# Kernel tuning notes

Hardware: AMD Instinct MI355X
Metric: run time of the kernel (lower is better)

## Reference

```python
import jax, jax.numpy as jnp
import numpy as np

N_NODES = 50000
N_EDGES = 600000
D_IN = 128      # input_dim
D_EDGE = 128    # edge_dim
GAMMA, ZETA = -0.1, 1.1  # hard-concrete stretch params


def _spectral_norm(w):
    # torch spectral_norm divides weight by its top singular value
    s = np.linalg.svd(w, compute_uv=False)[0]
    return w / s


def setup_inputs() -> dict:
    key = jax.random.key(0)
    ks = jax.random.split(key, 8)
    node_feat = jax.random.normal(ks[0], (N_NODES, D_IN), dtype=jnp.float32)
    edge_index = jax.random.randint(ks[1], (2, N_EDGES), 0, N_NODES, dtype=jnp.int64)
    rng = np.random.default_rng(0)
    # kaiming-normal init then spectral normalization (applied once at setup)
    def kaiming(fan_in, shape):
        return (rng.standard_normal(shape) * np.sqrt(2.0 / fan_in)).astype(np.float32)
    W1 = jnp.asarray(_spectral_norm(kaiming(2 * D_IN + 1, (D_EDGE, 2 * D_IN + 1))))
    W2 = jnp.asarray(_spectral_norm(kaiming(D_EDGE, (D_EDGE, D_EDGE))))
    W3 = jnp.asarray(_spectral_norm(kaiming(D_EDGE, (1, D_EDGE))))
    b1 = jnp.zeros((D_EDGE,), jnp.float32)
    b2 = jnp.zeros((D_EDGE,), jnp.float32)
    b3 = jnp.zeros((1,), jnp.float32)
    return {"node_feat": node_feat, "edge_index": edge_index,
            "W1": W1, "b1": b1, "W2": W2, "b2": b2, "W3": W3, "b3": b3}


def reference(node_feat, edge_index, W1, b1, W2, b2, W3, b3):
    # L2-normalize node features
    nf = node_feat / (jnp.linalg.norm(node_feat, axis=-1, keepdims=True) + 1e-8)
    src, tgt = edge_index[0], edge_index[1]
    hs = nf[src]                      # [E, D_IN] gather
    ht = nf[tgt]                      # [E, D_IN] gather
    dist = jnp.linalg.norm(hs - ht, axis=-1)  # [E]
    edge_features = jnp.concatenate([hs, ht, dist[:, None]], axis=-1)  # [E, 2D+1]
    h = jax.nn.relu(edge_features @ W1.T + b1)
    h = jax.nn.relu(h @ W2.T + b2)
    logAlpha = (h @ W3.T + b3).squeeze(-1)    # [E]
    # hard-concrete deterministic (l0_test) gate
    edge_weights = jnp.clip(jax.nn.sigmoid(logAlpha) * (ZETA - GAMMA) + GAMMA, 0.0, 1.0)
    return edge_weights, logAlpha
```

## Files before the change

### kernel.cpp

```cpp
#include <hip/hip_runtime.h>


#define E_TOT 600000
#define NN    50000
#define DIN   128

typedef short bf16x8 __attribute__((ext_vector_type(8)));
typedef float f32x4  __attribute__((ext_vector_type(4)));

union FragU { uint4 q; unsigned int u[4]; bf16x8 v; };

__device__ __forceinline__ unsigned int f2bf(float x) {
  unsigned int b = __float_as_uint(x);
  return ((b + 0x7fffu + ((b >> 16) & 1u)) >> 16) & 0xffffu;
}

__global__ __launch_bounds__(256) void k_norm(const float* __restrict__ nf,
                                              unsigned short* __restrict__ nfb) {
  const int wv = threadIdx.x >> 6, l = threadIdx.x & 63;
  const int h = l >> 5, r = l & 31;
  const int node = blockIdx.x * 8 + wv * 2 + h;
  const float4* row = (const float4*)(nf + (size_t)node * DIN);
  float4 v = row[r];
  float ss = v.x * v.x + v.y * v.y + v.z * v.z + v.w * v.w;
  #pragma unroll
  for (int msk = 1; msk < 32; msk <<= 1) ss += __shfl_xor(ss, msk);
  const float inv = 1.0f / (sqrtf(ss) + 1e-8f);
  uint2 o;
  o.x = f2bf(v.x * inv) | (f2bf(v.y * inv) << 16);
  o.y = f2bf(v.z * inv) | (f2bf(v.w * inv) << 16);
  ((uint2*)(nfb + (size_t)node * DIN))[r] = o;
}

__global__ __launch_bounds__(256) void k_prep(const float* __restrict__ W1,
                                              const float* __restrict__ W2,
                                              unsigned int* __restrict__ B1,
                                              unsigned int* __restrict__ B2) {
  const int id = blockIdx.x * 256 + threadIdx.x;
  if (id < 16384) {
    const int dw = id & 3, lane = (id >> 2) & 63, nt = (id >> 8) & 7, s = id >> 11;
    const int n = nt * 16 + (lane & 15);
    const int k0 = (lane >> 4) * 8 + s * 32 + dw * 2;
    B1[id] = f2bf(W1[n * 257 + k0]) | (f2bf(W1[n * 257 + k0 + 1]) << 16);
  } else {
    const int i2 = id - 16384;
    const int dw = i2 & 3, lane = (i2 >> 2) & 63, nt = (i2 >> 8) & 7, s = i2 >> 11;
    const int n = nt * 16 + (lane & 15);
    const int k0 = (lane >> 4) * 8 + s * 32 + dw * 2;
    B2[i2] = f2bf(W2[n * 128 + k0]) | (f2bf(W2[n * 128 + k0 + 1]) << 16);
  }
}

__global__ __launch_bounds__(256, 4) void k_main(
    const unsigned short* __restrict__ nfb, const int* __restrict__ ei,
    const unsigned int* __restrict__ B1, const unsigned int* __restrict__ B2,
    const float* __restrict__ W1, const float* __restrict__ b1,
    const float* __restrict__ b2, const float* __restrict__ W3,
    const float* __restrict__ b3, float* __restrict__ out) {
  __shared__ unsigned int lds[2048 + 4 * 1024];
  const int tid = threadIdx.x;
  const int wv = tid >> 6, l = tid & 63, m = l & 15, a = l >> 4;
  char* sHb = (char*)(lds + 2048) + wv * 4096;

  bool is64 = true;
  #pragma unroll
  for (int w = 1; w < 64; w += 2) is64 = is64 && (ei[w] == 0);

  const int e = blockIdx.x * 64 + wv * 16 + m;
  int nsrc, ntgt;
  if (is64) { nsrc = ei[2 * e]; ntgt = ei[2 * (E_TOT + e)]; }
  else      { nsrc = ei[e];     ntgt = ei[E_TOT + e]; }
  nsrc = min(max(nsrc, 0), NN - 1);
  ntgt = min(max(ntgt, 0), NN - 1);

  const uint4* rs = (const uint4*)(nfb + (size_t)nsrc * DIN);
  const uint4* rt = (const uint4*)(nfb + (size_t)ntgt * DIN);
  uint4 hsv[4], htv[4];
  #pragma unroll
  for (int s = 0; s < 4; ++s) { hsv[s] = rs[a + 4 * s]; htv[s] = rt[a + 4 * s]; }

  float dp = 0.f;
  #pragma unroll
  for (int i = 0; i < 4; ++i) {
    const unsigned int* hu = (const unsigned int*)&hsv[i];
    const unsigned int* tu = (const unsigned int*)&htv[i];
    #pragma unroll
    for (int j = 0; j < 4; ++j) {
      float h0 = __uint_as_float(hu[j] << 16), t0 = __uint_as_float(tu[j] << 16);
      float h1v = __uint_as_float(hu[j] & 0xffff0000u), t1v = __uint_as_float(tu[j] & 0xffff0000u);
      float d0 = h0 - t0, d1 = h1v - t1v;
      dp = fmaf(d0, d0, dp);
      dp = fmaf(d1, d1, dp);
    }
  }
  dp += __shfl_xor(dp, 16);
  dp += __shfl_xor(dp, 32);
  const float dist = sqrtf(dp);
  float dist_r[4];
  #pragma unroll
  for (int r = 0; r < 4; ++r) dist_r[r] = __shfl(dist, a * 4 + r);

  f32x4 acc[8];
  #pragma unroll
  for (int nt = 0; nt < 8; ++nt) acc[nt] = (f32x4){0.f, 0.f, 0.f, 0.f};

  const uint4* g1 = (const uint4*)B1;
  const uint4* g2 = (const uint4*)B2;
  uint4* sB = (uint4*)lds;
  uint4 n0 = g1[tid], n1 = g1[tid + 256];

  #pragma unroll
  for (int st = 0; st < 12; ++st) {
    __syncthreads();
    sB[tid] = n0; sB[tid + 256] = n1;
    __syncthreads();
    if (st < 11) {
      const int s2 = st + 1;
      if (s2 < 8) { n0 = g1[s2 * 512 + tid]; n1 = g1[s2 * 512 + tid + 256]; }
      else        { const int s3 = s2 - 8;
                    n0 = g2[s3 * 512 + tid]; n1 = g2[s3 * 512 + tid + 256]; }
    }

    FragU af;
    if (st < 4)      af.q = hsv[st];
    else if (st < 8) af.q = htv[st - 4];
    else {
      const int s2 = st - 8;
      const int col = 16 * a + 64 * s2;
      af.q = *(const uint4*)(sHb + m * 256 + (col ^ ((m & 7) << 4)));
    }

    #pragma unroll
    for (int nt = 0; nt < 8; ++nt) {
      FragU bfr; bfr.q = sB[nt * 64 + l];
      acc[nt] = __builtin_amdgcn_mfma_f32_16x16x32_bf16(af.v, bfr.v, acc[nt], 0, 0, 0);
    }

    if (st == 7) {
      #pragma unroll
      for (int nt = 0; nt < 8; ++nt) {
        const int n = nt * 16 + m;
        const float b1v = b1[n];
        const float w1l = W1[n * 257 + 256];
        #pragma unroll
        for (int r = 0; r < 4; ++r) {
          const int row = 4 * a + r;
          float v = acc[nt][r] + b1v + w1l * dist_r[r];
          v = fmaxf(v, 0.f);
          *(unsigned short*)(sHb + row * 256 + ((n * 2) ^ ((row & 7) << 4))) =
              (unsigned short)f2bf(v);
        }
        acc[nt] = (f32x4){0.f, 0.f, 0.f, 0.f};
      }
    }
  }

  float part[4] = {0.f, 0.f, 0.f, 0.f};
  #pragma unroll
  for (int nt = 0; nt < 8; ++nt) {
    const int n = nt * 16 + m;
    const float b2v = b2[n];
    const float w3v = W3[n];
    #pragma unroll
    for (int r = 0; r < 4; ++r) {
      const float h2 = fmaxf(acc[nt][r] + b2v, 0.f);
      part[r] = fmaf(h2, w3v, part[r]);
    }
  }
  #pragma unroll
  for (int r = 0; r < 4; ++r) {
    part[r] += __shfl_xor(part[r], 1);
    part[r] += __shfl_xor(part[r], 2);
    part[r] += __shfl_xor(part[r], 4);
    part[r] += __shfl_xor(part[r], 8);
  }
  if (m == 0) {
    const float b3v = b3[0];
    #pragma unroll
    for (int r = 0; r < 4; ++r) {
      const int eo = blockIdx.x * 64 + wv * 16 + a * 4 + r;
      const float la = part[r] + b3v;
      const float sg = 1.f / (1.f + __expf(-la));
      out[eo] = fminf(fmaxf(sg * 1.2f - 0.1f, 0.f), 1.f);
      out[E_TOT + eo] = la;
    }
  }
}

extern "C" void kernel_launch(void* const* d_in, const int* in_sizes, int n_in,
                              void* d_out, int out_size, void* d_ws, size_t ws_size,
                              hipStream_t stream) {
  const float* node_feat = (const float*)d_in[0];
  const int*   edge_idx  = (const int*)d_in[1];
  const float* W1 = (const float*)d_in[2];
  const float* b1 = (const float*)d_in[3];
  const float* W2 = (const float*)d_in[4];
  const float* b2 = (const float*)d_in[5];
  const float* W3 = (const float*)d_in[6];
  const float* b3 = (const float*)d_in[7];
  float* out = (float*)d_out;

  unsigned char* ws = (unsigned char*)d_ws;
  unsigned short* nfb = (unsigned short*)(ws);
  unsigned int*   B1  = (unsigned int*)(ws + 12800000);
  unsigned int*   B2  = (unsigned int*)(ws + 12800000 + 65536);

  hipLaunchKernelGGL(k_norm, dim3(6250), dim3(256), 0, stream, node_feat, nfb);
  hipLaunchKernelGGL(k_prep, dim3(96), dim3(256), 0, stream, W1, W2, B1, B2);
  hipLaunchKernelGGL(k_main, dim3(9375), dim3(256), 0, stream,
                     nfb, edge_idx, B1, B2, W1, b1, b2, W3, b3, out);
}
```

Before: 202.2 us.

## Process two edge tiles per wave with async double-buffered weight staging

Each wave now handles 32 edges (two 16-row MFMA tiles), so every staged weight fragment in LDS feeds twice as many MFMAs. Weight staging switches from register round-trips to global_load_lds async copies into a double buffer, which drops one barrier per stage. The norm and weight-prep kernels are merged into a single launch, and the 64-bit index detection becomes a wave vote. In exchange, register and LDS use grow, occupancy is bounded at 3 blocks, and the grid halves with a tail guard.

```diff
diff --git a/kernel.cpp b/kernel.cpp
--- a/kernel.cpp
+++ b/kernel.cpp
@@ -15,125 +15,156 @@
   return ((b + 0x7fffu + ((b >> 16) & 1u)) >> 16) & 0xffffu;
 }
 
-__global__ __launch_bounds__(256) void k_norm(const float* __restrict__ nf,
-                                              unsigned short* __restrict__ nfb) {
-  const int wv = threadIdx.x >> 6, l = threadIdx.x & 63;
-  const int h = l >> 5, r = l & 31;
-  const int node = blockIdx.x * 8 + wv * 2 + h;
-  const float4* row = (const float4*)(nf + (size_t)node * DIN);
-  float4 v = row[r];
-  float ss = v.x * v.x + v.y * v.y + v.z * v.z + v.w * v.w;
-  #pragma unroll
-  for (int msk = 1; msk < 32; msk <<= 1) ss += __shfl_xor(ss, msk);
-  const float inv = 1.0f / (sqrtf(ss) + 1e-8f);
-  uint2 o;
-  o.x = f2bf(v.x * inv) | (f2bf(v.y * inv) << 16);
-  o.y = f2bf(v.z * inv) | (f2bf(v.w * inv) << 16);
-  ((uint2*)(nfb + (size_t)node * DIN))[r] = o;
-}
-
-__global__ __launch_bounds__(256) void k_prep(const float* __restrict__ W1,
-                                              const float* __restrict__ W2,
-                                              unsigned int* __restrict__ B1,
-                                              unsigned int* __restrict__ B2) {
-  const int id = blockIdx.x * 256 + threadIdx.x;
-  if (id < 16384) {
-    const int dw = id & 3, lane = (id >> 2) & 63, nt = (id >> 8) & 7, s = id >> 11;
-    const int n = nt * 16 + (lane & 15);
-    const int k0 = (lane >> 4) * 8 + s * 32 + dw * 2;
-    B1[id] = f2bf(W1[n * 257 + k0]) | (f2bf(W1[n * 257 + k0 + 1]) << 16);
+__device__ __forceinline__ void async_cp16(const uint4* g, uint4* l) {
+  __builtin_amdgcn_global_load_lds((const __attribute__((address_space(1))) void*)g,
+                                   (__attribute__((address_space(3))) void*)l, 16, 0, 0);
+}
+
+__global__ __launch_bounds__(256) void k_pre(const float* __restrict__ nf,
+                                             const float* __restrict__ W1,
+                                             const float* __restrict__ W2,
+                                             unsigned short* __restrict__ nfb,
+                                             unsigned int* __restrict__ B1,
+                                             unsigned int* __restrict__ B2) {
+  if (blockIdx.x < 6250) {
+    const int wv = threadIdx.x >> 6, l = threadIdx.x & 63;
+    const int h = l >> 5, r = l & 31;
+    const int node = blockIdx.x * 8 + wv * 2 + h;
+    const float4* row = (const float4*)(nf + (size_t)node * DIN);
+    float4 v = row[r];
+    float ss = v.x * v.x + v.y * v.y + v.z * v.z + v.w * v.w;
+    #pragma unroll
+    for (int msk = 1; msk < 32; msk <<= 1) ss += __shfl_xor(ss, msk);
+    const float inv = 1.0f / (sqrtf(ss) + 1e-8f);
+    uint2 o;
+    o.x = f2bf(v.x * inv) | (f2bf(v.y * inv) << 16);
+    o.y = f2bf(v.z * inv) | (f2bf(v.w * inv) << 16);
+    ((uint2*)(nfb + (size_t)node * DIN))[r] = o;
   } else {
-    const int i2 = id - 16384;
-    const int dw = i2 & 3, lane = (i2 >> 2) & 63, nt = (i2 >> 8) & 7, s = i2 >> 11;
-    const int n = nt * 16 + (lane & 15);
-    const int k0 = (lane >> 4) * 8 + s * 32 + dw * 2;
-    B2[i2] = f2bf(W2[n * 128 + k0]) | (f2bf(W2[n * 128 + k0 + 1]) << 16);
-  }
-}
-
-__global__ __launch_bounds__(256, 4) void k_main(
+    const int id = (blockIdx.x - 6250) * 256 + threadIdx.x;
+    if (id < 16384) {
+      const int dw = id & 3, lane = (id >> 2) & 63, nt = (id >> 8) & 7, s = id >> 11;
+      const int n = nt * 16 + (lane & 15);
+      const int k0 = (lane >> 4) * 8 + s * 32 + dw * 2;
+      B1[id] = f2bf(W1[n * 257 + k0]) | (f2bf(W1[n * 257 + k0 + 1]) << 16);
+    } else {
+      const int i2 = id - 16384;
+      const int dw = i2 & 3, lane = (i2 >> 2) & 63, nt = (i2 >> 8) & 7, s = i2 >> 11;
+      const int n = nt * 16 + (lane & 15);
+      const int k0 = (lane >> 4) * 8 + s * 32 + dw * 2;
+      B2[i2] = f2bf(W2[n * 128 + k0]) | (f2bf(W2[n * 128 + k0 + 1]) << 16);
+    }
+  }
+}
+
+__global__ __launch_bounds__(256, 3) void k_main(
     const unsigned short* __restrict__ nfb, const int* __restrict__ ei,
     const unsigned int* __restrict__ B1, const unsigned int* __restrict__ B2,
     const float* __restrict__ W1, const float* __restrict__ b1,
     const float* __restrict__ b2, const float* __restrict__ W3,
     const float* __restrict__ b3, float* __restrict__ out) {
-  __shared__ unsigned int lds[2048 + 4 * 1024];
+  __shared__ unsigned int lds[4096 + 4 * 2048];
   const int tid = threadIdx.x;
   const int wv = tid >> 6, l = tid & 63, m = l & 15, a = l >> 4;
-  char* sHb = (char*)(lds + 2048) + wv * 4096;
-
-  bool is64 = true;
-  #pragma unroll
-  for (int w = 1; w < 64; w += 2) is64 = is64 && (ei[w] == 0);
-
-  const int e = blockIdx.x * 64 + wv * 16 + m;
-  int nsrc, ntgt;
-  if (is64) { nsrc = ei[2 * e]; ntgt = ei[2 * (E_TOT + e)]; }
-  else      { nsrc = ei[e];     ntgt = ei[E_TOT + e]; }
-  nsrc = min(max(nsrc, 0), NN - 1);
-  ntgt = min(max(ntgt, 0), NN - 1);
-
-  const uint4* rs = (const uint4*)(nfb + (size_t)nsrc * DIN);
-  const uint4* rt = (const uint4*)(nfb + (size_t)ntgt * DIN);
-  uint4 hsv[4], htv[4];
-  #pragma unroll
-  for (int s = 0; s < 4; ++s) { hsv[s] = rs[a + 4 * s]; htv[s] = rt[a + 4 * s]; }
-
-  float dp = 0.f;
-  #pragma unroll
-  for (int i = 0; i < 4; ++i) {
-    const unsigned int* hu = (const unsigned int*)&hsv[i];
-    const unsigned int* tu = (const unsigned int*)&htv[i];
-    #pragma unroll
-    for (int j = 0; j < 4; ++j) {
-      float h0 = __uint_as_float(hu[j] << 16), t0 = __uint_as_float(tu[j] << 16);
-      float h1v = __uint_as_float(hu[j] & 0xffff0000u), t1v = __uint_as_float(tu[j] & 0xffff0000u);
-      float d0 = h0 - t0, d1 = h1v - t1v;
-      dp = fmaf(d0, d0, dp);
-      dp = fmaf(d1, d1, dp);
-    }
-  }
-  dp += __shfl_xor(dp, 16);
-  dp += __shfl_xor(dp, 32);
-  const float dist = sqrtf(dp);
-  float dist_r[4];
-  #pragma unroll
-  for (int r = 0; r < 4; ++r) dist_r[r] = __shfl(dist, a * 4 + r);
-
-  f32x4 acc[8];
-  #pragma unroll
-  for (int nt = 0; nt < 8; ++nt) acc[nt] = (f32x4){0.f, 0.f, 0.f, 0.f};
+  char* sH0 = (char*)(lds + 4096) + wv * 8192;
+  char* sH1 = sH0 + 4096;
+
+  const int w0 = ei[l];
+  const bool is64 = __all((l & 1) == 0 || w0 == 0);
+
+  const int e0 = blockIdx.x * 128 + wv * 32 + m;
+  const int ec0 = min(e0, E_TOT - 1);
+  const int ec1 = min(e0 + 16, E_TOT - 1);
+  int ns0, nt0_, ns1, nt1_;
+  if (is64) { ns0 = ei[2 * ec0]; nt0_ = ei[2 * (E_TOT + ec0)];
+              ns1 = ei[2 * ec1]; nt1_ = ei[2 * (E_TOT + ec1)]; }
+  else      { ns0 = ei[ec0];     nt0_ = ei[E_TOT + ec0];
+              ns1 = ei[ec1];     nt1_ = ei[E_TOT + ec1]; }
+  ns0 = min(max(ns0, 0), NN - 1);  nt0_ = min(max(nt0_, 0), NN - 1);
+  ns1 = min(max(ns1, 0), NN - 1);  nt1_ = min(max(nt1_, 0), NN - 1);
+
+  const uint4* rs0 = (const uint4*)(nfb + (size_t)ns0 * DIN);
+  const uint4* rt0 = (const uint4*)(nfb + (size_t)nt0_ * DIN);
+  const uint4* rs1 = (const uint4*)(nfb + (size_t)ns1 * DIN);
+  const uint4* rt1 = (const uint4*)(nfb + (size_t)nt1_ * DIN);
+  uint4 hsv0[4], htv0[4], hsv1[4], htv1[4];
+  #pragma unroll
+  for (int s = 0; s < 4; ++s) {
+    hsv0[s] = rs0[a + 4 * s]; htv0[s] = rt0[a + 4 * s];
+    hsv1[s] = rs1[a + 4 * s]; htv1[s] = rt1[a + 4 * s];
+  }
+
+  float dist_r0[4], dist_r1[4];
+  {
+    float dp0 = 0.f, dp1 = 0.f;
+    #pragma unroll
+    for (int i = 0; i < 4; ++i) {
+      const unsigned int* h0u = (const unsigned int*)&hsv0[i];
+      const unsigned int* t0u = (const unsigned int*)&htv0[i];
+      const unsigned int* h1u = (const unsigned int*)&hsv1[i];
+      const unsigned int* t1u = (const unsigned int*)&htv1[i];
+      #pragma unroll
+      for (int j = 0; j < 4; ++j) {
+        float dlo = __uint_as_float(h0u[j] << 16) - __uint_as_float(t0u[j] << 16);
+        float dhi = __uint_as_float(h0u[j] & 0xffff0000u) - __uint_as_float(t0u[j] & 0xffff0000u);
+        dp0 = fmaf(dlo, dlo, dp0); dp0 = fmaf(dhi, dhi, dp0);
+        float elo = __uint_as_float(h1u[j] << 16) - __uint_as_float(t1u[j] << 16);
+        float ehi = __uint_as_float(h1u[j] & 0xffff0000u) - __uint_as_float(t1u[j] & 0xffff0000u);
+        dp1 = fmaf(elo, elo, dp1); dp1 = fmaf(ehi, ehi, dp1);
+      }
+    }
+    dp0 += __shfl_xor(dp0, 16); dp0 += __shfl_xor(dp0, 32);
+    dp1 += __shfl_xor(dp1, 16); dp1 += __shfl_xor(dp1, 32);
+    const float d0 = sqrtf(dp0), d1 = sqrtf(dp1);
+    #pragma unroll
+    for (int r = 0; r < 4; ++r) {
+      dist_r0[r] = __shfl(d0, a * 4 + r);
+      dist_r1[r] = __shfl(d1, a * 4 + r);
+    }
+  }
+
+  f32x4 acc0[8], acc1[8];
+  #pragma unroll
+  for (int nt = 0; nt < 8; ++nt) {
+    acc0[nt] = (f32x4){0.f, 0.f, 0.f, 0.f};
+    acc1[nt] = (f32x4){0.f, 0.f, 0.f, 0.f};
+  }
 
   const uint4* g1 = (const uint4*)B1;
   const uint4* g2 = (const uint4*)B2;
-  uint4* sB = (uint4*)lds;
-  uint4 n0 = g1[tid], n1 = g1[tid + 256];
+  uint4* sB0 = (uint4*)lds;
+  uint4* sB1b = sB0 + 512;
+
+  #define STAGE(c) do {                                                      \
+    const uint4* gs_ = ((c) < 8) ? (g1 + (c) * 512) : (g2 + ((c) - 8) * 512);\
+    uint4* db_ = (((c) & 1) ? sB1b : sB0);                                   \
+    async_cp16(gs_ + wv * 64 + l, db_ + wv * 64);                            \
+    async_cp16(gs_ + 256 + wv * 64 + l, db_ + 256 + wv * 64);                \
+  } while (0)
+
+  STAGE(0);
+  __syncthreads();
 
   #pragma unroll
   for (int st = 0; st < 12; ++st) {
-    __syncthreads();
-    sB[tid] = n0; sB[tid + 256] = n1;
-    __syncthreads();
-    if (st < 11) {
-      const int s2 = st + 1;
-      if (s2 < 8) { n0 = g1[s2 * 512 + tid]; n1 = g1[s2 * 512 + tid + 256]; }
-      else        { const int s3 = s2 - 8;
-                    n0 = g2[s3 * 512 + tid]; n1 = g2[s3 * 512 + tid + 256]; }
-    }
-
-    FragU af;
-    if (st < 4)      af.q = hsv[st];
-    else if (st < 8) af.q = htv[st - 4];
+    if (st < 11) STAGE(st + 1);
+
+    FragU af0, af1;
+    if (st < 4)      { af0.q = hsv0[st];     af1.q = hsv1[st]; }
+    else if (st < 8) { af0.q = htv0[st - 4]; af1.q = htv1[st - 4]; }
     else {
       const int s2 = st - 8;
-      const int col = 16 * a + 64 * s2;
-      af.q = *(const uint4*)(sHb + m * 256 + (col ^ ((m & 7) << 4)));
-    }
-
+      const int col = (16 * a + 64 * s2) ^ ((m & 7) << 4);
+      af0.q = *(const uint4*)(sH0 + m * 256 + col);
+      af1.q = *(const uint4*)(sH1 + m * 256 + col);
+    }
+
+    const uint4* sB = (st & 1) ? sB1b : sB0;
     #pragma unroll
     for (int nt = 0; nt < 8; ++nt) {
       FragU bfr; bfr.q = sB[nt * 64 + l];
-      acc[nt] = __builtin_amdgcn_mfma_f32_16x16x32_bf16(af.v, bfr.v, acc[nt], 0, 0, 0);
+      acc0[nt] = __builtin_amdgcn_mfma_f32_16x16x32_bf16(af0.v, bfr.v, acc0[nt], 0, 0, 0);
+      acc1[nt] = __builtin_amdgcn_mfma_f32_16x16x32_bf16(af1.v, bfr.v, acc1[nt], 0, 0, 0);
     }
 
     if (st == 7) {
@@ -145,17 +176,20 @@
         #pragma unroll
         for (int r = 0; r < 4; ++r) {
           const int row = 4 * a + r;
-          float v = acc[nt][r] + b1v + w1l * dist_r[r];
-          v = fmaxf(v, 0.f);
-          *(unsigned short*)(sHb + row * 256 + ((n * 2) ^ ((row & 7) << 4))) =
-              (unsigned short)f2bf(v);
+          const int cb = (2 * n) ^ ((row & 7) << 4);
+          float v0 = fmaxf(acc0[nt][r] + b1v + w1l * dist_r0[r], 0.f);
+          float v1 = fmaxf(acc1[nt][r] + b1v + w1l * dist_r1[r], 0.f);
+          *(unsigned short*)(sH0 + row * 256 + cb) = (unsigned short)f2bf(v0);
+          *(unsigned short*)(sH1 + row * 256 + cb) = (unsigned short)f2bf(v1);
         }
-        acc[nt] = (f32x4){0.f, 0.f, 0.f, 0.f};
+        acc0[nt] = (f32x4){0.f, 0.f, 0.f, 0.f};
+        acc1[nt] = (f32x4){0.f, 0.f, 0.f, 0.f};
       }
     }
-  }
-
-  float part[4] = {0.f, 0.f, 0.f, 0.f};
+    __syncthreads();
+  }
+
+  float p0[4] = {0.f, 0.f, 0.f, 0.f}, p1[4] = {0.f, 0.f, 0.f, 0.f};
   #pragma unroll
   for (int nt = 0; nt < 8; ++nt) {
     const int n = nt * 16 + m;
@@ -163,26 +197,32 @@
     const float w3v = W3[n];
     #pragma unroll
     for (int r = 0; r < 4; ++r) {
-      const float h2 = fmaxf(acc[nt][r] + b2v, 0.f);
-      part[r] = fmaf(h2, w3v, part[r]);
+      p0[r] = fmaf(fmaxf(acc0[nt][r] + b2v, 0.f), w3v, p0[r]);
+      p1[r] = fmaf(fmaxf(acc1[nt][r] + b2v, 0.f), w3v, p1[r]);
     }
   }
   #pragma unroll
   for (int r = 0; r < 4; ++r) {
-    part[r] += __shfl_xor(part[r], 1);
-    part[r] += __shfl_xor(part[r], 2);
-    part[r] += __shfl_xor(part[r], 4);
-    part[r] += __shfl_xor(part[r], 8);
+    #pragma unroll
+    for (int msk = 1; msk < 16; msk <<= 1) {
+      p0[r] += __shfl_xor(p0[r], msk);
+      p1[r] += __shfl_xor(p1[r], msk);
+    }
   }
   if (m == 0) {
     const float b3v = b3[0];
     #pragma unroll
-    for (int r = 0; r < 4; ++r) {
-      const int eo = blockIdx.x * 64 + wv * 16 + a * 4 + r;
-      const float la = part[r] + b3v;
-      const float sg = 1.f / (1.f + __expf(-la));
-      out[eo] = fminf(fmaxf(sg * 1.2f - 0.1f, 0.f), 1.f);
-      out[E_TOT + eo] = la;
+    for (int t = 0; t < 2; ++t) {
+      #pragma unroll
+      for (int r = 0; r < 4; ++r) {
+        const int eo = blockIdx.x * 128 + wv * 32 + t * 16 + a * 4 + r;
+        if (eo < E_TOT) {
+          const float la = (t ? p1[r] : p0[r]) + b3v;
+          const float sg = 1.f / (1.f + __expf(-la));
+          out[eo] = fminf(fmaxf(sg * 1.2f - 0.1f, 0.f), 1.f);
+          out[E_TOT + eo] = la;
+        }
+      }
     }
   }
 }
@@ -205,8 +245,8 @@
   unsigned int*   B1  = (unsigned int*)(ws + 12800000);
   unsigned int*   B2  = (unsigned int*)(ws + 12800000 + 65536);
 
-  hipLaunchKernelGGL(k_norm, dim3(6250), dim3(256), 0, stream, node_feat, nfb);
-  hipLaunchKernelGGL(k_prep, dim3(96), dim3(256), 0, stream, W1, W2, B1, B2);
-  hipLaunchKernelGGL(k_main, dim3(9375), dim3(256), 0, stream,
+  hipLaunchKernelGGL(k_pre, dim3(6346), dim3(256), 0, stream,
+                     node_feat, W1, W2, nfb, B1, B2);
+  hipLaunchKernelGGL(k_main, dim3(4688), dim3(256), 0, stream,
                      nfb, edge_idx, B1, B2, W1, b1, b2, W3, b3, out);
 }
```

New measurement: 191.6 us. -5.2%, faster.
